# Kernel optimization log

Hardware: AMD Instinct MI355X
Metric: run time of the kernel (lower is better)

Reference implementation:

```python
import jax, jax.numpy as jnp
import numpy as np

T, B, V, H, C = 256, 25, 32000, 1024, 2  # time steps, step_size, vocab, hidden, classes

def _xavier(key, shape):
    fan_in, fan_out = shape
    std = (2.0 / (fan_in + fan_out)) ** 0.5
    return std * jax.random.normal(key, shape, dtype=jnp.float32)

def setup_inputs() -> dict:
    key = jax.random.key(0)
    k0, k1, k2, k3 = jax.random.split(key, 4)
    X = jax.random.normal(k0, (T, B, V), dtype=jnp.float32)
    W_xh = _xavier(k1, (V, H))
    W_hh = _xavier(k2, (H, H))
    b_h = jnp.zeros((H,), dtype=jnp.float32)
    fc_w = _xavier(k3, (H, C))  # nn.Linear(num_hiddens, 2) weight (stored transposed here)
    fc_b = jnp.zeros((C,), dtype=jnp.float32)
    return {"X": X, "W_xh": W_xh, "W_hh": W_hh, "b_h": b_h, "fc_w": fc_w, "fc_b": fc_b}

def reference(X, W_xh, W_hh, b_h, fc_w, fc_b):
    # state: [step_size, H], initialized to zeros as in get_init_state_per_batch
    h0 = jnp.zeros((X.shape[1], W_hh.shape[0]), dtype=X.dtype)

    def step(h, x_t):
        # tanh(X @ W_xh + state @ W_hh + b_h)
        h_new = jnp.tanh(x_t @ W_xh + h @ W_hh + b_h)
        return h_new, None

    hT, _ = jax.lax.scan(step, h0, X)  # recurrence over T timesteps
    pooled = hT.mean(axis=0, keepdims=True)      # [1, H]
    logits = pooled @ fc_w + fc_b                # [1, 2]
    return jax.nn.softmax(logits, axis=1)
```

## Files before the change

kernel.cpp:

```cpp
#include <hip/hip_runtime.h>

#define T_STEPS 256
#define BATCH   25
#define VOCAB   32000
#define HID     1024

typedef _Float16 half8  __attribute__((ext_vector_type(8)));
typedef float    floatx4  __attribute__((ext_vector_type(4)));
typedef float    floatx16 __attribute__((ext_vector_type(16)));

#define OFF_BT  (26214400)
#define OFF_HA  (26214400 + 65536000)
#define OFF_HB  (26214400 + 65536000 + 65536)
#define OFF_CNT (26214400 + 65536000 + 131072)

__global__ __launch_bounds__(256) void k_transpose(const float* __restrict__ W,
                                                   _Float16* __restrict__ Bt,
                                                   int* __restrict__ cnt) {
    if (blockIdx.x == 0 && blockIdx.y == 0 && threadIdx.x == 0) *cnt = 0;
    __shared__ _Float16 tile[64][72];
    const int k0 = blockIdx.x * 64;
    const int n0 = blockIdx.y * 64;
    const int t  = threadIdx.x;
    #pragma unroll
    for (int i = 0; i < 4; ++i) {
        int s  = t + i * 256;
        int r  = s >> 4;
        int c4 = (s & 15) * 4;
        const float4 v = *(const float4*)(W + (size_t)(k0 + r) * HID + n0 + c4);
        tile[r][c4 + 0] = (_Float16)v.x;
        tile[r][c4 + 1] = (_Float16)v.y;
        tile[r][c4 + 2] = (_Float16)v.z;
        tile[r][c4 + 3] = (_Float16)v.w;
    }
    __syncthreads();
    #pragma unroll
    for (int i = 0; i < 2; ++i) {
        int s  = t + i * 256;
        int nr = s >> 3;
        int k8 = (s & 7) * 8;
        half8 h;
        #pragma unroll
        for (int j = 0; j < 8; ++j) h[j] = tile[k8 + j][nr];
        *(half8*)(Bt + (size_t)(n0 + nr) * VOCAB + k0 + k8) = h;
    }
}

__global__ __launch_bounds__(256) void k_gemm(const float* __restrict__ X,
                                              const _Float16* __restrict__ Bt,
                                              float* __restrict__ P) {
    const int bid = blockIdx.x;
    const int c   = bid & 7;
    const int j   = bid >> 3;
    const int mt  = (j >> 3) * 8 + c;
    const int nt  = j & 7;
    if (mt >= 50) return;
    const int m0 = mt * 128, n0 = nt * 128;

    __shared__ _Float16 sA[4096];
    __shared__ _Float16 sB[4096];

    const int tid  = threadIdx.x;
    const int lane = tid & 63;
    const int wv   = tid >> 6;
    const int wm   = wv >> 1;
    const int wn   = wv & 1;

    floatx4 acc[4][4];
    #pragma unroll
    for (int i = 0; i < 4; ++i)
        #pragma unroll
        for (int jj = 0; jj < 4; ++jj) acc[i][jj] = 0.0f;

    for (int kc = 0; kc < VOCAB / 32; ++kc) {
        const int k0 = kc * 32;
        __syncthreads();
        #pragma unroll
        for (int r = 0; r < 2; ++r) {
            int s  = tid + r * 256;
            int m  = s >> 2;
            int ko = s & 3;
            const float4* gp = (const float4*)(X + (size_t)(m0 + m) * VOCAB + k0 + ko * 8);
            float4 v0 = gp[0], v1 = gp[1];
            half8 ha;
            ha[0] = (_Float16)v0.x; ha[1] = (_Float16)v0.y;
            ha[2] = (_Float16)v0.z; ha[3] = (_Float16)v0.w;
            ha[4] = (_Float16)v1.x; ha[5] = (_Float16)v1.y;
            ha[6] = (_Float16)v1.z; ha[7] = (_Float16)v1.w;
            int ti = m >> 4;
            int li = (ko << 4) | (m & 15);
            *(half8*)&sA[ti * 512 + li * 8] = ha;
            half8 hb = *(const half8*)(Bt + (size_t)(n0 + m) * VOCAB + k0 + ko * 8);
            *(half8*)&sB[ti * 512 + li * 8] = hb;
        }
        __syncthreads();
        half8 af[4], bf[4];
        #pragma unroll
        for (int i = 0; i < 4; ++i) af[i] = *(const half8*)&sA[(wm * 4 + i) * 512 + lane * 8];
        #pragma unroll
        for (int i = 0; i < 4; ++i) bf[i] = *(const half8*)&sB[(wn * 4 + i) * 512 + lane * 8];
        #pragma unroll
        for (int i = 0; i < 4; ++i)
            #pragma unroll
            for (int jj = 0; jj < 4; ++jj)
                acc[i][jj] = __builtin_amdgcn_mfma_f32_16x16x32_f16(af[i], bf[jj], acc[i][jj], 0, 0, 0);
    }

    const int quad = lane >> 4, col = lane & 15;
    #pragma unroll
    for (int i = 0; i < 4; ++i) {
        int mg = m0 + wm * 64 + i * 16 + quad * 4;
        #pragma unroll
        for (int jj = 0; jj < 4; ++jj) {
            int ng = n0 + wn * 64 + jj * 16 + col;
            #pragma unroll
            for (int r = 0; r < 4; ++r)
                P[(size_t)(mg + r) * HID + ng] = acc[i][jj][r];
        }
    }
}

__device__ __forceinline__ void gbar(int* cnt, int target) {
    __syncthreads();
    if (threadIdx.x == 0) {
        __threadfence();
        atomicAdd(cnt, 1);
        while (__hip_atomic_load(cnt, __ATOMIC_ACQUIRE, __HIP_MEMORY_SCOPE_AGENT) < target) {
            __builtin_amdgcn_s_sleep(1);
        }
    }
    __syncthreads();
    __threadfence();
}

__global__ __launch_bounds__(64) void k_rec(const float* __restrict__ P,
                                            const float* __restrict__ Whh,
                                            const float* __restrict__ bh,
                                            const float* __restrict__ fcw,
                                            const float* __restrict__ fcb,
                                            _Float16* __restrict__ hA,
                                            _Float16* __restrict__ hB,
                                            float* __restrict__ out,
                                            int* __restrict__ cnt) {
    const int wg   = blockIdx.x;
    const int lane = threadIdx.x;
    const int n0   = wg * 32;

    __shared__ _Float16 smem[32768];

    {
        const int n  = lane & 31;
        const int kh = lane >> 5;
        for (int kk = 0; kk < 64; ++kk) {
            half8 h;
            #pragma unroll
            for (int jj = 0; jj < 8; ++jj) {
                int k = kk * 16 + kh * 8 + jj;
                h[jj] = (_Float16)Whh[(size_t)k * HID + n0 + n];
            }
            *(half8*)&smem[kk * 512 + lane * 8] = h;
        }
    }

    {
        int gid = wg * 64 + lane;
        float4 z = {0.f, 0.f, 0.f, 0.f};
        *(float4*)(hA + gid * 16)     = z;
        *(float4*)(hA + gid * 16 + 8) = z;
    }

    int barNum = 0;
    const _Float16* R  = hA;
    _Float16*       Wb = hB;
    const int m  = lane & 31;
    const int kh = lane >> 5;

    for (int t = 0; t < T_STEPS; ++t) {
        gbar(cnt, (++barNum) * 32);

        floatx16 c0 = 0.0f, c1 = 0.0f;
        #pragma unroll 4
        for (int kk = 0; kk < 64; kk += 2) {
            half8 a0 = *(const half8*)(R + (size_t)m * HID + kk * 16 + kh * 8);
            half8 b0 = *(const half8*)&smem[kk * 512 + lane * 8];
            half8 a1 = *(const half8*)(R + (size_t)m * HID + (kk + 1) * 16 + kh * 8);
            half8 b1 = *(const half8*)&smem[(kk + 1) * 512 + lane * 8];
            c0 = __builtin_amdgcn_mfma_f32_32x32x16_f16(a0, b0, c0, 0, 0, 0);
            c1 = __builtin_amdgcn_mfma_f32_32x32x16_f16(a1, b1, c1, 0, 0, 0);
        }

        const float* Pt = P + (size_t)t * BATCH * HID;
        #pragma unroll
        for (int r = 0; r < 16; ++r) {
            int row = (r & 3) + 8 * (r >> 2) + 4 * kh;
            if (row < BATCH) {
                int colg  = n0 + m;
                float pre = c0[r] + c1[r] + Pt[row * HID + colg] + bh[colg];
                Wb[(size_t)row * HID + colg] = (_Float16)tanhf(pre);
            }
        }
        _Float16* tmp = Wb; Wb = (_Float16*)R; R = tmp;
    }

    gbar(cnt, (++barNum) * 32);

    if (wg == 0) {
        float l0 = 0.f, l1 = 0.f;
        for (int col = lane; col < HID; col += 64) {
            float s = 0.f;
            for (int b = 0; b < BATCH; ++b) s += (float)R[(size_t)b * HID + col];
            float pooled = s * (1.0f / BATCH);
            l0 += pooled * fcw[col * 2 + 0];
            l1 += pooled * fcw[col * 2 + 1];
        }
        #pragma unroll
        for (int off = 32; off > 0; off >>= 1) {
            l0 += __shfl_down(l0, off);
            l1 += __shfl_down(l1, off);
        }
        if (lane == 0) {
            l0 += fcb[0]; l1 += fcb[1];
            float mx = fmaxf(l0, l1);
            float e0 = __expf(l0 - mx), e1 = __expf(l1 - mx);
            float inv = 1.0f / (e0 + e1);
            out[0] = e0 * inv;
            out[1] = e1 * inv;
        }
    }
}

extern "C" void kernel_launch(void* const* d_in, const int* in_sizes, int n_in,
                              void* d_out, int out_size, void* d_ws, size_t ws_size,
                              hipStream_t stream) {
    const float* X   = (const float*)d_in[0];
    const float* Wxh = (const float*)d_in[1];
    const float* Whh = (const float*)d_in[2];
    const float* bh  = (const float*)d_in[3];
    const float* fcw = (const float*)d_in[4];
    const float* fcb = (const float*)d_in[5];

    char* ws = (char*)d_ws;
    float*    P   = (float*)ws;
    _Float16* Bt  = (_Float16*)(ws + OFF_BT);
    _Float16* hA  = (_Float16*)(ws + OFF_HA);
    _Float16* hB  = (_Float16*)(ws + OFF_HB);
    int*      cnt = (int*)(ws + OFF_CNT);

    hipLaunchKernelGGL(k_transpose, dim3(500, 16), dim3(256), 0, stream, Wxh, Bt, cnt);
    hipLaunchKernelGGL(k_gemm, dim3(448), dim3(256), 0, stream, X, Bt, P);
    hipLaunchKernelGGL(k_rec, dim3(32), dim3(64), 0, stream,
                       P, Whh, bh, fcw, fcb, hA, hB, (float*)d_out, cnt);
}
```

Baseline: 5.821 ms.

## Split recurrence into per-batch chains with register-resident W_hh and local flags

```diff
diff --git a/kernel.cpp b/kernel.cpp
--- a/kernel.cpp
+++ b/kernel.cpp
@@ -5,19 +5,25 @@
 #define VOCAB   32000
 #define HID     1024
 
+#define NPART   8
+#define NCOLS   128
+#define NCHAIN  BATCH
+#define NWG     (NCHAIN * NPART)
+
 typedef _Float16 half8  __attribute__((ext_vector_type(8)));
+typedef _Float16 half2v __attribute__((ext_vector_type(2)));
 typedef float    floatx4  __attribute__((ext_vector_type(4)));
-typedef float    floatx16 __attribute__((ext_vector_type(16)));
 
 #define OFF_BT  (26214400)
-#define OFF_HA  (26214400 + 65536000)
-#define OFF_HB  (26214400 + 65536000 + 65536)
-#define OFF_CNT (26214400 + 65536000 + 131072)
+#define OFF_H0  (26214400 + 65536000)
+#define OFF_H1  (OFF_H0 + 65536)
+#define OFF_FLG (OFF_H1 + 51200)
 
 __global__ __launch_bounds__(256) void k_transpose(const float* __restrict__ W,
                                                    _Float16* __restrict__ Bt,
-                                                   int* __restrict__ cnt) {
-    if (blockIdx.x == 0 && blockIdx.y == 0 && threadIdx.x == 0) *cnt = 0;
+                                                   int* __restrict__ flags) {
+    if (blockIdx.x == 0 && blockIdx.y == 0 && threadIdx.x < NWG)
+        flags[threadIdx.x] = 0;
     __shared__ _Float16 tile[64][72];
     const int k0 = blockIdx.x * 64;
     const int n0 = blockIdx.y * 64;
@@ -120,111 +126,127 @@
     }
 }
 
-__device__ __forceinline__ void gbar(int* cnt, int target) {
-    __syncthreads();
-    if (threadIdx.x == 0) {
-        __threadfence();
-        atomicAdd(cnt, 1);
-        while (__hip_atomic_load(cnt, __ATOMIC_ACQUIRE, __HIP_MEMORY_SCOPE_AGENT) < target) {
-            __builtin_amdgcn_s_sleep(1);
-        }
-    }
-    __syncthreads();
-    __threadfence();
-}
-
-__global__ __launch_bounds__(64) void k_rec(const float* __restrict__ P,
-                                            const float* __restrict__ Whh,
-                                            const float* __restrict__ bh,
-                                            const float* __restrict__ fcw,
-                                            const float* __restrict__ fcb,
-                                            _Float16* __restrict__ hA,
-                                            _Float16* __restrict__ hB,
-                                            float* __restrict__ out,
-                                            int* __restrict__ cnt) {
-    const int wg   = blockIdx.x;
-    const int lane = threadIdx.x;
-    const int n0   = wg * 32;
-
-    __shared__ _Float16 smem[32768];
-
+static __device__ __forceinline__ float dot2(half2v a, half2v b, float c) {
+#if __has_builtin(__builtin_amdgcn_fdot2)
+    return __builtin_amdgcn_fdot2(a, b, c, false);
+#else
+    return c + (float)a[0] * (float)b[0] + (float)a[1] * (float)b[1];
+#endif
+}
+
+__global__ __launch_bounds__(256, 1) void k_rec(const float* __restrict__ P,
+                                                const float* __restrict__ Whh,
+                                                const float* __restrict__ bh,
+                                                const float* __restrict__ fcw,
+                                                const float* __restrict__ fcb,
+                                                _Float16* __restrict__ H0,
+                                                _Float16* __restrict__ H1,
+                                                float* __restrict__ out,
+                                                int* __restrict__ flags) {
+    const int wg  = blockIdx.x;
+    const int b   = wg >> 3;
+    const int j   = wg & 7;
+    const int n0  = j * NCOLS;
+    const int tid = threadIdx.x;
+    const int col = tid & (NCOLS - 1);
+    const int kh  = tid >> 7;
+    const int kbase = kh * 512;
+
+    __shared__ alignas(16) _Float16 hsm[HID];
+    __shared__ float red[NCOLS];
+
+    half8 wreg[64];
     {
-        const int n  = lane & 31;
-        const int kh = lane >> 5;
+        const float* wp = Whh + (size_t)kbase * HID + n0 + col;
+        #pragma unroll
         for (int kk = 0; kk < 64; ++kk) {
             half8 h;
             #pragma unroll
-            for (int jj = 0; jj < 8; ++jj) {
-                int k = kk * 16 + kh * 8 + jj;
-                h[jj] = (_Float16)Whh[(size_t)k * HID + n0 + n];
-            }
-            *(half8*)&smem[kk * 512 + lane * 8] = h;
-        }
-    }
-
-    {
-        int gid = wg * 64 + lane;
-        float4 z = {0.f, 0.f, 0.f, 0.f};
-        *(float4*)(hA + gid * 16)     = z;
-        *(float4*)(hA + gid * 16 + 8) = z;
-    }
-
-    int barNum = 0;
-    const _Float16* R  = hA;
-    _Float16*       Wb = hB;
-    const int m  = lane & 31;
-    const int kh = lane >> 5;
+            for (int q = 0; q < 8; ++q)
+                h[q] = (_Float16)wp[(size_t)(kk * 8 + q) * HID];
+            wreg[kk] = h;
+        }
+    }
+
+    const float bhreg = bh[n0 + col];
+    int* flg = flags + b * NPART;
 
     for (int t = 0; t < T_STEPS; ++t) {
-        gbar(cnt, (++barNum) * 32);
-
-        floatx16 c0 = 0.0f, c1 = 0.0f;
-        #pragma unroll 4
-        for (int kk = 0; kk < 64; kk += 2) {
-            half8 a0 = *(const half8*)(R + (size_t)m * HID + kk * 16 + kh * 8);
-            half8 b0 = *(const half8*)&smem[kk * 512 + lane * 8];
-            half8 a1 = *(const half8*)(R + (size_t)m * HID + (kk + 1) * 16 + kh * 8);
-            half8 b1 = *(const half8*)&smem[(kk + 1) * 512 + lane * 8];
-            c0 = __builtin_amdgcn_mfma_f32_32x32x16_f16(a0, b0, c0, 0, 0, 0);
-            c1 = __builtin_amdgcn_mfma_f32_32x32x16_f16(a1, b1, c1, 0, 0, 0);
-        }
-
-        const float* Pt = P + (size_t)t * BATCH * HID;
-        #pragma unroll
-        for (int r = 0; r < 16; ++r) {
-            int row = (r & 3) + 8 * (r >> 2) + 4 * kh;
-            if (row < BATCH) {
-                int colg  = n0 + m;
-                float pre = c0[r] + c1[r] + Pt[row * HID + colg] + bh[colg];
-                Wb[(size_t)row * HID + colg] = (_Float16)tanhf(pre);
-            }
-        }
-        _Float16* tmp = Wb; Wb = (_Float16*)R; R = tmp;
-    }
-
-    gbar(cnt, (++barNum) * 32);
+        float pval = P[((size_t)t * BATCH + b) * HID + n0 + col];
+        float a0 = 0.f, a1 = 0.f, a2 = 0.f, a3 = 0.f;
+
+        if (t > 0) {
+            const _Float16* hin = ((t & 1) ? H1 : H0) + (size_t)b * HID;
+            if (tid < NPART && tid != j) {
+                while (__hip_atomic_load(&flg[tid], __ATOMIC_ACQUIRE,
+                                         __HIP_MEMORY_SCOPE_AGENT) < t) {}
+            }
+            __syncthreads();
+            __threadfence();
+            *(uint2*)&hsm[tid * 4] = *(const uint2*)&hin[tid * 4];
+            __syncthreads();
+
+            #pragma unroll
+            for (int kk = 0; kk < 64; ++kk) {
+                half8 hv = *(const half8*)&hsm[kbase + kk * 8];
+                half8 w  = wreg[kk];
+                a0 = dot2(__builtin_shufflevector(hv, hv, 0, 1),
+                          __builtin_shufflevector(w,  w,  0, 1), a0);
+                a1 = dot2(__builtin_shufflevector(hv, hv, 2, 3),
+                          __builtin_shufflevector(w,  w,  2, 3), a1);
+                a2 = dot2(__builtin_shufflevector(hv, hv, 4, 5),
+                          __builtin_shufflevector(w,  w,  4, 5), a2);
+                a3 = dot2(__builtin_shufflevector(hv, hv, 6, 7),
+                          __builtin_shufflevector(w,  w,  6, 7), a3);
+            }
+        }
+
+        float acc = (a0 + a1) + (a2 + a3);
+        if (kh) red[col] = acc;
+        __syncthreads();
+        if (!kh) {
+            float s = acc + red[col] + pval + bhreg;
+            _Float16* Hout = (((t + 1) & 1) ? H1 : H0) + (size_t)b * HID;
+            Hout[n0 + col] = (_Float16)tanhf(s);
+        }
+        __syncthreads();
+        if (tid == 0) {
+            __threadfence();
+            __hip_atomic_store(&flg[j], t + 1, __ATOMIC_RELEASE,
+                               __HIP_MEMORY_SCOPE_AGENT);
+        }
+    }
 
     if (wg == 0) {
-        float l0 = 0.f, l1 = 0.f;
-        for (int col = lane; col < HID; col += 64) {
-            float s = 0.f;
-            for (int b = 0; b < BATCH; ++b) s += (float)R[(size_t)b * HID + col];
-            float pooled = s * (1.0f / BATCH);
-            l0 += pooled * fcw[col * 2 + 0];
-            l1 += pooled * fcw[col * 2 + 1];
-        }
-        #pragma unroll
-        for (int off = 32; off > 0; off >>= 1) {
-            l0 += __shfl_down(l0, off);
-            l1 += __shfl_down(l1, off);
-        }
-        if (lane == 0) {
-            l0 += fcb[0]; l1 += fcb[1];
-            float mx = fmaxf(l0, l1);
-            float e0 = __expf(l0 - mx), e1 = __expf(l1 - mx);
-            float inv = 1.0f / (e0 + e1);
-            out[0] = e0 * inv;
-            out[1] = e1 * inv;
+        if (tid < NWG) {
+            while (__hip_atomic_load(&flags[tid], __ATOMIC_ACQUIRE,
+                                     __HIP_MEMORY_SCOPE_AGENT) < T_STEPS) {}
+        }
+        __syncthreads();
+        __threadfence();
+        if (tid < 64) {
+            const _Float16* R = H0;
+            float l0 = 0.f, l1 = 0.f;
+            for (int c = tid; c < HID; c += 64) {
+                float s = 0.f;
+                for (int bb = 0; bb < BATCH; ++bb) s += (float)R[(size_t)bb * HID + c];
+                float pooled = s * (1.0f / BATCH);
+                l0 += pooled * fcw[c * 2 + 0];
+                l1 += pooled * fcw[c * 2 + 1];
+            }
+            #pragma unroll
+            for (int off = 32; off > 0; off >>= 1) {
+                l0 += __shfl_down(l0, off);
+                l1 += __shfl_down(l1, off);
+            }
+            if (tid == 0) {
+                l0 += fcb[0]; l1 += fcb[1];
+                float mx = fmaxf(l0, l1);
+                float e0 = __expf(l0 - mx), e1 = __expf(l1 - mx);
+                float inv = 1.0f / (e0 + e1);
+                out[0] = e0 * inv;
+                out[1] = e1 * inv;
+            }
         }
     }
 }
@@ -242,12 +264,12 @@
     char* ws = (char*)d_ws;
     float*    P   = (float*)ws;
     _Float16* Bt  = (_Float16*)(ws + OFF_BT);
-    _Float16* hA  = (_Float16*)(ws + OFF_HA);
-    _Float16* hB  = (_Float16*)(ws + OFF_HB);
-    int*      cnt = (int*)(ws + OFF_CNT);
-
-    hipLaunchKernelGGL(k_transpose, dim3(500, 16), dim3(256), 0, stream, Wxh, Bt, cnt);
+    _Float16* H0  = (_Float16*)(ws + OFF_H0);
+    _Float16* H1  = (_Float16*)(ws + OFF_H1);
+    int*      flg = (int*)(ws + OFF_FLG);
+
+    hipLaunchKernelGGL(k_transpose, dim3(500, 16), dim3(256), 0, stream, Wxh, Bt, flg);
     hipLaunchKernelGGL(k_gemm, dim3(448), dim3(256), 0, stream, X, Bt, P);
-    hipLaunchKernelGGL(k_rec, dim3(32), dim3(64), 0, stream,
-                       P, Whh, bh, fcw, fcb, hA, hB, (float*)d_out, cnt);
-}
+    hipLaunchKernelGGL(k_rec, dim3(NWG), dim3(256), 0, stream,
+                       P, Whh, bh, fcw, fcb, H0, H1, (float*)d_out, flg);
+}
```

After: 7.463 ms. +28.2%, slower.
